# Performance work log

Hardware: AMD Instinct MI355X
Metric: run time of the kernel (lower is better)

The kernel has to match this reference:

```python
import jax, jax.numpy as jnp
import numpy as np


def setup_inputs() -> dict:
    key = jax.random.key(0)
    k1, k2, k3 = jax.random.split(key, 3)
    N = 100000
    E = 1600000
    d = 128
    indices = jax.random.randint(k1, (2, E), 0, N, dtype=jnp.int64)
    values = jax.random.uniform(k2, (E,), dtype=jnp.float32)
    b = jax.random.normal(k3, (N, d), dtype=jnp.float32)
    return {"indices": indices, "values": values, "b": b, "N": N, "layer_id": 0}


def reference(indices, values, b, N, layer_id):
    # Sparse COO matmul: out[r] = sum_{e: row[e]==r} values[e] * b[col[e]]
    row = indices[0]  # [E]
    col = indices[1]  # [E]
    contrib = values[:, None] * b[col]  # [E, d] gathered + scaled edge messages
    out = jax.ops.segment_sum(contrib, row, num_segments=N)  # [N, d]
    return out
```

## Files before the change

kernel.cpp:

```cpp
#include <hip/hip_runtime.h>


#define DIM 128
#define RPB 32
#define BLK 128
#define STAGE 768
#define CAP (STAGE + 7 * RPB)
#define NCH 256
#define MAXNB 4096

__device__ __forceinline__ unsigned short f2bf(float f) {
    unsigned u = __float_as_uint(f);
    return (unsigned short)((u + 0x7FFFu + ((u >> 16) & 1u)) >> 16);
}
__device__ __forceinline__ float4 ldbf4(const char* p) {
    ushort4 h = *reinterpret_cast<const ushort4*>(p);
    float4 r;
    r.x = __uint_as_float((unsigned)h.x << 16);
    r.y = __uint_as_float((unsigned)h.y << 16);
    r.z = __uint_as_float((unsigned)h.z << 16);
    r.w = __uint_as_float((unsigned)h.w << 16);
    return r;
}

__global__ __launch_bounds__(256) void spmm_atomic_kernel(
    const int* __restrict__ rows, const int* __restrict__ cols,
    const float* __restrict__ vals, const float* __restrict__ b,
    float* __restrict__ out, int E)
{
    long long t = (long long)blockIdx.x * blockDim.x + threadIdx.x;
    int e = (int)(t >> 5);
    if (e >= E) return;
    int j = ((int)t & 31) * 4;
    int r = rows[e]; int c = cols[e]; float v = vals[e];
    const float4 bv = *reinterpret_cast<const float4*>(b + (size_t)c * DIM + j);
    float* o = out + (size_t)r * DIM + j;
    atomicAdd(o + 0, v * bv.x);
    atomicAdd(o + 1, v * bv.y);
    atomicAdd(o + 2, v * bv.z);
    atomicAdd(o + 3, v * bv.w);
}

__global__ __launch_bounds__(256) void conv_count_kernel(
    const float* __restrict__ b, unsigned short* __restrict__ bh, int n4,
    const int* __restrict__ rows, int* __restrict__ ccount, int E)
{
    for (int i = blockIdx.x * blockDim.x + threadIdx.x; i < n4;
         i += gridDim.x * blockDim.x) {
        float4 v = reinterpret_cast<const float4*>(b)[i];
        ushort4 h;
        h.x = f2bf(v.x); h.y = f2bf(v.y); h.z = f2bf(v.z); h.w = f2bf(v.w);
        reinterpret_cast<ushort4*>(bh)[i] = h;
    }
    __shared__ int hist[MAXNB];
    for (int i = threadIdx.x; i < MAXNB; i += 256) hist[i] = 0;
    __syncthreads();
    int chunk = (E + NCH - 1) / NCH;
    int s = blockIdx.x * chunk;
    int e = min(s + chunk, E);
    for (int i = s + threadIdx.x; i < e; i += 256)
        atomicAdd(&hist[rows[i] >> 5], 1);
    __syncthreads();
    for (int i = threadIdx.x; i < MAXNB; i += 256)
        if (hist[i]) atomicAdd(&ccount[i], hist[i]);
}

__global__ __launch_bounds__(1024) void coarse_scan_kernel(
    const int* __restrict__ ccount, int* __restrict__ coffsets,
    int* __restrict__ ccursor, int NB, int E)
{
    __shared__ int s[1024];
    int t = threadIdx.x;
    int i0 = 4 * t;
    int a0 = (i0     < NB) ? ccount[i0]     : 0;
    int a1 = (i0 + 1 < NB) ? ccount[i0 + 1] : 0;
    int a2 = (i0 + 2 < NB) ? ccount[i0 + 2] : 0;
    int a3 = (i0 + 3 < NB) ? ccount[i0 + 3] : 0;
    int sum4 = a0 + a1 + a2 + a3;
    s[t] = sum4;
    __syncthreads();
    for (int off = 1; off < 1024; off <<= 1) {
        int x = (t >= off) ? s[t - off] : 0;
        __syncthreads();
        s[t] += x;
        __syncthreads();
    }
    int excl = s[t] - sum4;
    if (i0     < NB) { coffsets[i0]     = excl;                ccursor[i0]     = excl; }
    if (i0 + 1 < NB) { coffsets[i0 + 1] = excl + a0;           ccursor[i0 + 1] = excl + a0; }
    if (i0 + 2 < NB) { coffsets[i0 + 2] = excl + a0 + a1;      ccursor[i0 + 2] = excl + a0 + a1; }
    if (i0 + 3 < NB) { coffsets[i0 + 3] = excl + a0 + a1 + a2; ccursor[i0 + 3] = excl + a0 + a1 + a2; }
    if (t == 0) coffsets[NB] = E;
}

__global__ __launch_bounds__(256) void partition_kernel(
    const int* __restrict__ rows, const int* __restrict__ cols,
    const float* __restrict__ vals, int* __restrict__ ccursor,
    unsigned long long* __restrict__ pairs, int E)
{
    __shared__ int hist[MAXNB];
    __shared__ int base[MAXNB];
    for (int i = threadIdx.x; i < MAXNB; i += 256) hist[i] = 0;
    __syncthreads();
    int chunk = (E + NCH - 1) / NCH;
    int s = blockIdx.x * chunk;
    int e = min(s + chunk, E);
    for (int i = s + threadIdx.x; i < e; i += 256)
        atomicAdd(&hist[rows[i] >> 5], 1);
    __syncthreads();
    for (int i = threadIdx.x; i < MAXNB; i += 256) {
        int c = hist[i];
        base[i] = c ? atomicAdd(&ccursor[i], c) : 0;
        hist[i] = 0;
    }
    __syncthreads();
    for (int i = s + threadIdx.x; i < e; i += 256) {
        int r = rows[i];
        int cb = r >> 5;
        int pos = base[cb] + atomicAdd(&hist[cb], 1);
        unsigned long long p =
            ((unsigned long long)(unsigned)__float_as_int(vals[i]) << 32) |
            (unsigned)((cols[i] << 5) | (r & (RPB - 1)));
        pairs[pos] = p;
    }
}

template<bool BF16>
__global__ __launch_bounds__(BLK) void bucket_accum_kernel(
    const int* __restrict__ coffsets,
    const unsigned long long* __restrict__ pairs,
    const void* __restrict__ bmat, float* __restrict__ out, int N)
{
    __shared__ int2 svec[CAP];
    __shared__ int fcnt[RPB];
    __shared__ int foff[RPB + 1];
    __shared__ int stmp[RPB];

    int cb = blockIdx.x;
    int cstart = coffsets[cb];
    int Mtot = coffsets[cb + 1] - cstart;
    int M = min(Mtot, STAGE);
    int t = threadIdx.x;

    unsigned long long ep0 = 0, ep1 = 0, ep2 = 0, ep3 = 0, ep4 = 0, ep5 = 0;
    {
        const unsigned long long* p = pairs + cstart;
        if (t         < M) ep0 = p[t];
        if (t + 128   < M) ep1 = p[t + 128];
        if (t + 256   < M) ep2 = p[t + 256];
        if (t + 384   < M) ep3 = p[t + 384];
        if (t + 512   < M) ep4 = p[t + 512];
        if (t + 640   < M) ep5 = p[t + 640];
    }
    for (int i = t; i < CAP; i += BLK) svec[i] = make_int2(0, 0);
    if (t < RPB) fcnt[t] = 0;
    __syncthreads();

    if (t         < M) atomicAdd(&fcnt[(int)(ep0 & (RPB - 1))], 1);
    if (t + 128   < M) atomicAdd(&fcnt[(int)(ep1 & (RPB - 1))], 1);
    if (t + 256   < M) atomicAdd(&fcnt[(int)(ep2 & (RPB - 1))], 1);
    if (t + 384   < M) atomicAdd(&fcnt[(int)(ep3 & (RPB - 1))], 1);
    if (t + 512   < M) atomicAdd(&fcnt[(int)(ep4 & (RPB - 1))], 1);
    if (t + 640   < M) atomicAdd(&fcnt[(int)(ep5 & (RPB - 1))], 1);
    __syncthreads();

    int pc = 0;
    if (t < RPB) { pc = (fcnt[t] + 7) & ~7; stmp[t] = pc; }
    __syncthreads();
    for (int off = 1; off < RPB; off <<= 1) {
        int x = 0;
        if (t < RPB && t >= off) x = stmp[t - off];
        __syncthreads();
        if (t < RPB) stmp[t] += x;
        __syncthreads();
    }
    if (t < RPB) {
        int excl = stmp[t] - pc;
        foff[t] = excl;
        fcnt[t] = excl;
    }
    if (t == RPB - 1) foff[RPB] = stmp[t];
    __syncthreads();

#define RANK_WRITE(EP, OFS)                                                  \
    if (t + (OFS) < M) {                                                     \
        unsigned lo = (unsigned)(EP & 0xffffffffu);                          \
        int pos = atomicAdd(&fcnt[(int)(lo & (RPB - 1))], 1);                \
        svec[pos] = make_int2((int)((lo & 0xffffffe0u) << (BF16 ? 3 : 4)),   \
                              (int)(EP >> 32));                              \
    }
    RANK_WRITE(ep0, 0)   RANK_WRITE(ep1, 128) RANK_WRITE(ep2, 256)
    RANK_WRITE(ep3, 384) RANK_WRITE(ep4, 512) RANK_WRITE(ep5, 640)
#undef RANK_WRITE
    __syncthreads();

    int wid  = t >> 6;
    int lane = t & 63;
    int h    = lane >> 5;
    int sub  = lane & 31;
    const char* blh = (const char*)bmat + sub * (BF16 ? 8 : 16);

#define GATHER(DST, OFS)                                                     \
    if constexpr (BF16) DST = ldbf4(blh + (OFS));                            \
    else DST = *reinterpret_cast<const float4*>(blh + (OFS));

#define FMA4(EV, CV)                                                         \
    { float v = __int_as_float(EV.y);                                        \
      acc.x = fmaf(v, CV.x, acc.x); acc.y = fmaf(v, CV.y, acc.y);            \
      acc.z = fmaf(v, CV.z, acc.z); acc.w = fmaf(v, CV.w, acc.w); }

    for (int j = 0; j < 16; ++j) {
        int rl = wid * 16 + j;
        int rg = cb * RPB + rl;
        if (rg >= N) break;
        float4 acc = make_float4(0.f, 0.f, 0.f, 0.f);
        int ks = foff[rl], ke = foff[rl + 1];
        if (ks < ke) {
            int2 e0 = svec[ks + h],     e1 = svec[ks + 2 + h];
            int2 e2 = svec[ks + 4 + h], e3 = svec[ks + 6 + h];
            float4 c0, c1, c2, c3;
            GATHER(c0, e0.x) GATHER(c1, e1.x) GATHER(c2, e2.x) GATHER(c3, e3.x)
            for (int k = ks + 8; k < ke; k += 8) {
                int2 f0 = svec[k + h],     f1 = svec[k + 2 + h];
                int2 f2 = svec[k + 4 + h], f3 = svec[k + 6 + h];
                float4 d0, d1, d2, d3;
                GATHER(d0, f0.x) GATHER(d1, f1.x) GATHER(d2, f2.x) GATHER(d3, f3.x)
                __builtin_amdgcn_sched_barrier(0);
                FMA4(e0, c0) FMA4(e1, c1) FMA4(e2, c2) FMA4(e3, c3)
                e0 = f0; e1 = f1; e2 = f2; e3 = f3;
                c0 = d0; c1 = d1; c2 = d2; c3 = d3;
            }
            FMA4(e0, c0) FMA4(e1, c1) FMA4(e2, c2) FMA4(e3, c3)
        }
        if (h == 0) {
            for (int q = STAGE; q < Mtot; ++q) {
                unsigned long long p = pairs[cstart + q];
                if ((int)(p & (RPB - 1)) == rl) {
                    unsigned lo = (unsigned)(p & 0xffffffffu);
                    float v = __int_as_float((int)(p >> 32));
                    float4 bv;
                    GATHER(bv, (int)((lo & 0xffffffe0u) << (BF16 ? 3 : 4)))
                    acc.x = fmaf(v, bv.x, acc.x); acc.y = fmaf(v, bv.y, acc.y);
                    acc.z = fmaf(v, bv.z, acc.z); acc.w = fmaf(v, bv.w, acc.w);
                }
            }
        }
        acc.x += __shfl_xor(acc.x, 32);
        acc.y += __shfl_xor(acc.y, 32);
        acc.z += __shfl_xor(acc.z, 32);
        acc.w += __shfl_xor(acc.w, 32);
        if (h == 0)
            *reinterpret_cast<float4*>(out + (size_t)rg * DIM + sub * 4) = acc;
    }
#undef FMA4
#undef GATHER
}

extern "C" void kernel_launch(void* const* d_in, const int* in_sizes, int n_in,
                              void* d_out, int out_size, void* d_ws, size_t ws_size,
                              hipStream_t stream)
{
    const int*   indices = (const int*)d_in[0];
    const float* vals    = (const float*)d_in[1];
    const float* b       = (const float*)d_in[2];
    float*       out     = (float*)d_out;

    const int E = in_sizes[1];
    const int N = in_sizes[2] / DIM;
    const int* rows = indices;
    const int* cols = indices + E;

    const int NB = (N + RPB - 1) / RPB;

    size_t pairs_bytes = (size_t)E * 8;
    size_t bh_bytes    = (size_t)N * DIM * 2;
    size_t cnt_bytes   = ((size_t)NB * 3 + 1) * 4;
    size_t needed_f32  = pairs_bytes + cnt_bytes;
    size_t needed_bf16 = pairs_bytes + bh_bytes + cnt_bytes;

    if (ws_size < needed_f32 || NB > MAXNB || NB < 1 || E < 1) {
        hipMemsetAsync(d_out, 0, (size_t)out_size * sizeof(float), stream);
        if (E >= 1) {
            const long long total = (long long)E * 32;
            const int grid = (int)((total + 255) / 256);
            spmm_atomic_kernel<<<grid, 256, 0, stream>>>(rows, cols, vals, b, out, E);
        }
        return;
    }

    const bool use_bf16 = (ws_size >= needed_bf16);

    char* base = (char*)d_ws;
    unsigned long long* pairs = (unsigned long long*)base;
    size_t off = pairs_bytes;
    unsigned short* bh = nullptr;
    if (use_bf16) { bh = (unsigned short*)(base + off); off += bh_bytes; }
    int* ccount   = (int*)(base + off);
    int* coffsets = ccount + NB;
    int* ccursor  = coffsets + (NB + 1);

    hipMemsetAsync(ccount, 0, (size_t)NB * sizeof(int), stream);
    conv_count_kernel<<<NCH, 256, 0, stream>>>(
        b, bh, use_bf16 ? N * DIM / 4 : 0, rows, ccount, E);
    coarse_scan_kernel<<<1, 1024, 0, stream>>>(ccount, coffsets, ccursor, NB, E);
    partition_kernel<<<NCH, 256, 0, stream>>>(rows, cols, vals, ccursor, pairs, E);
    if (use_bf16)
        bucket_accum_kernel<true><<<NB, BLK, 0, stream>>>(coffsets, pairs, bh, out, N);
    else
        bucket_accum_kernel<false><<<NB, BLK, 0, stream>>>(coffsets, pairs, b, out, N);
}
```

Before: 152.3 us.

## Split edge partitioning into two-level radix scatter via superbuckets

Partitioning now runs in two passes: edges are first scattered into superbuckets of 1024 rows, then each superbucket is redistributed into 32-row buckets. The pair encoding widens the row field to 10 bits so the second pass can read the sub-bucket index. The aim is more local, better-coalesced scatter writes than a single scatter into thousands of buckets. The cost is an extra pass over the pair array, additional workspace, and an extra kernel launch.

```diff
diff --git a/kernel.cpp b/kernel.cpp
--- a/kernel.cpp
+++ b/kernel.cpp
@@ -7,7 +7,10 @@
 #define STAGE 768
 #define CAP (STAGE + 7 * RPB)
 #define NCH 256
+#define NCH1 1024
+#define PB2 8
 #define MAXNB 4096
+#define MAXNSB 128
 
 __device__ __forceinline__ unsigned short f2bf(float f) {
     unsigned u = __float_as_uint(f);
@@ -67,7 +70,7 @@
 
 __global__ __launch_bounds__(1024) void coarse_scan_kernel(
     const int* __restrict__ ccount, int* __restrict__ coffsets,
-    int* __restrict__ ccursor, int NB, int E)
+    int* __restrict__ ccursor, int* __restrict__ scursor, int NB, int E)
 {
     __shared__ int s[1024];
     int t = threadIdx.x;
@@ -90,10 +93,79 @@
     if (i0 + 1 < NB) { coffsets[i0 + 1] = excl + a0;           ccursor[i0 + 1] = excl + a0; }
     if (i0 + 2 < NB) { coffsets[i0 + 2] = excl + a0 + a1;      ccursor[i0 + 2] = excl + a0 + a1; }
     if (i0 + 3 < NB) { coffsets[i0 + 3] = excl + a0 + a1 + a2; ccursor[i0 + 3] = excl + a0 + a1 + a2; }
+    if ((i0 & 31) == 0 && i0 < NB) scursor[i0 >> 5] = excl;
     if (t == 0) coffsets[NB] = E;
 }
 
-__global__ __launch_bounds__(256) void partition_kernel(
+#define PACK(VAL, COL, ROW)                                                  \
+    (((unsigned long long)(unsigned)__float_as_int(VAL) << 32) |             \
+     (unsigned)(((COL) << 10) | ((ROW) & 1023)))
+
+__global__ __launch_bounds__(256) void partition1_kernel(
+    const int* __restrict__ rows, const int* __restrict__ cols,
+    const float* __restrict__ vals, int* __restrict__ scursor,
+    unsigned long long* __restrict__ pairs1, int E)
+{
+    __shared__ int hist[MAXNSB];
+    __shared__ int base[MAXNSB];
+    if (threadIdx.x < MAXNSB) hist[threadIdx.x] = 0;
+    __syncthreads();
+    int chunk = (E + NCH1 - 1) / NCH1;
+    int s = blockIdx.x * chunk;
+    int e = min(s + chunk, E);
+    for (int i = s + threadIdx.x; i < e; i += 256)
+        atomicAdd(&hist[rows[i] >> 10], 1);
+    __syncthreads();
+    if (threadIdx.x < MAXNSB) {
+        int c = hist[threadIdx.x];
+        base[threadIdx.x] = c ? atomicAdd(&scursor[threadIdx.x], c) : 0;
+        hist[threadIdx.x] = 0;
+    }
+    __syncthreads();
+    for (int i = s + threadIdx.x; i < e; i += 256) {
+        int r = rows[i];
+        int sb = r >> 10;
+        int pos = base[sb] + atomicAdd(&hist[sb], 1);
+        pairs1[pos] = PACK(vals[i], cols[i], r);
+    }
+}
+
+__global__ __launch_bounds__(256) void partition2_kernel(
+    const int* __restrict__ coffsets, int* __restrict__ ccursor,
+    const unsigned long long* __restrict__ pairs1,
+    unsigned long long* __restrict__ pairs2, int NB)
+{
+    int sb = blockIdx.x >> 3;
+    int q  = blockIdx.x & (PB2 - 1);
+    int b0 = sb * 32;
+    int b1 = min(b0 + 32, NB);
+    int sstart = coffsets[b0];
+    int len = coffsets[b1] - sstart;
+    int s = sstart + (int)((long long)len * q / PB2);
+    int e = sstart + (int)((long long)len * (q + 1) / PB2);
+
+    __shared__ int hist[32];
+    __shared__ int base[32];
+    if (threadIdx.x < 32) hist[threadIdx.x] = 0;
+    __syncthreads();
+    for (int i = s + threadIdx.x; i < e; i += 256)
+        atomicAdd(&hist[((unsigned)pairs1[i] >> 5) & 31], 1);
+    __syncthreads();
+    if (threadIdx.x < 32) {
+        int c = hist[threadIdx.x];
+        base[threadIdx.x] = c ? atomicAdd(&ccursor[b0 + threadIdx.x], c) : 0;
+        hist[threadIdx.x] = 0;
+    }
+    __syncthreads();
+    for (int i = s + threadIdx.x; i < e; i += 256) {
+        unsigned long long p = pairs1[i];
+        int sub = ((unsigned)p >> 5) & 31;
+        int pos = base[sub] + atomicAdd(&hist[sub], 1);
+        pairs2[pos] = p;
+    }
+}
+
+__global__ __launch_bounds__(256) void partition_single_kernel(
     const int* __restrict__ rows, const int* __restrict__ cols,
     const float* __restrict__ vals, int* __restrict__ ccursor,
     unsigned long long* __restrict__ pairs, int E)
@@ -118,10 +190,7 @@
         int r = rows[i];
         int cb = r >> 5;
         int pos = base[cb] + atomicAdd(&hist[cb], 1);
-        unsigned long long p =
-            ((unsigned long long)(unsigned)__float_as_int(vals[i]) << 32) |
-            (unsigned)((cols[i] << 5) | (r & (RPB - 1)));
-        pairs[pos] = p;
+        pairs[pos] = PACK(vals[i], cols[i], r);
     }
 }
 
@@ -156,12 +225,12 @@
     if (t < RPB) fcnt[t] = 0;
     __syncthreads();
 
-    if (t         < M) atomicAdd(&fcnt[(int)(ep0 & (RPB - 1))], 1);
-    if (t + 128   < M) atomicAdd(&fcnt[(int)(ep1 & (RPB - 1))], 1);
-    if (t + 256   < M) atomicAdd(&fcnt[(int)(ep2 & (RPB - 1))], 1);
-    if (t + 384   < M) atomicAdd(&fcnt[(int)(ep3 & (RPB - 1))], 1);
-    if (t + 512   < M) atomicAdd(&fcnt[(int)(ep4 & (RPB - 1))], 1);
-    if (t + 640   < M) atomicAdd(&fcnt[(int)(ep5 & (RPB - 1))], 1);
+    if (t         < M) atomicAdd(&fcnt[(int)(ep0 & 31u)], 1);
+    if (t + 128   < M) atomicAdd(&fcnt[(int)(ep1 & 31u)], 1);
+    if (t + 256   < M) atomicAdd(&fcnt[(int)(ep2 & 31u)], 1);
+    if (t + 384   < M) atomicAdd(&fcnt[(int)(ep3 & 31u)], 1);
+    if (t + 512   < M) atomicAdd(&fcnt[(int)(ep4 & 31u)], 1);
+    if (t + 640   < M) atomicAdd(&fcnt[(int)(ep5 & 31u)], 1);
     __syncthreads();
 
     int pc = 0;
@@ -185,8 +254,8 @@
 #define RANK_WRITE(EP, OFS)                                                  \
     if (t + (OFS) < M) {                                                     \
         unsigned lo = (unsigned)(EP & 0xffffffffu);                          \
-        int pos = atomicAdd(&fcnt[(int)(lo & (RPB - 1))], 1);                \
-        svec[pos] = make_int2((int)((lo & 0xffffffe0u) << (BF16 ? 3 : 4)),   \
+        int pos = atomicAdd(&fcnt[(int)(lo & 31u)], 1);                      \
+        svec[pos] = make_int2((int)((lo >> 10) << (BF16 ? 8 : 9)),           \
                               (int)(EP >> 32));                              \
     }
     RANK_WRITE(ep0, 0)   RANK_WRITE(ep1, 128) RANK_WRITE(ep2, 256)
@@ -235,11 +304,11 @@
         if (h == 0) {
             for (int q = STAGE; q < Mtot; ++q) {
                 unsigned long long p = pairs[cstart + q];
-                if ((int)(p & (RPB - 1)) == rl) {
+                if ((int)(p & 31u) == rl) {
                     unsigned lo = (unsigned)(p & 0xffffffffu);
                     float v = __int_as_float((int)(p >> 32));
                     float4 bv;
-                    GATHER(bv, (int)((lo & 0xffffffe0u) << (BF16 ? 3 : 4)))
+                    GATHER(bv, (int)((lo >> 10) << (BF16 ? 8 : 9)))
                     acc.x = fmaf(v, bv.x, acc.x); acc.y = fmaf(v, bv.y, acc.y);
                     acc.z = fmaf(v, bv.z, acc.z); acc.w = fmaf(v, bv.w, acc.w);
                 }
@@ -270,13 +339,15 @@
     const int* rows = indices;
     const int* cols = indices + E;
 
-    const int NB = (N + RPB - 1) / RPB;
+    const int NB  = (N + RPB - 1) / RPB;
+    const int NSB = (NB + 31) / 32;
 
     size_t pairs_bytes = (size_t)E * 8;
     size_t bh_bytes    = (size_t)N * DIM * 2;
-    size_t cnt_bytes   = ((size_t)NB * 3 + 1) * 4;
+    size_t cnt_bytes   = ((size_t)NB * 3 + 1 + NSB) * 4;
     size_t needed_f32  = pairs_bytes + cnt_bytes;
     size_t needed_bf16 = pairs_bytes + bh_bytes + cnt_bytes;
+    size_t needed_2lv  = needed_bf16 + pairs_bytes;
 
     if (ws_size < needed_f32 || NB > MAXNB || NB < 1 || E < 1) {
         hipMemsetAsync(d_out, 0, (size_t)out_size * sizeof(float), stream);
@@ -288,24 +359,37 @@
         return;
     }
 
-    const bool use_bf16 = (ws_size >= needed_bf16);
+    const bool use_bf16  = (ws_size >= needed_bf16);
+    const bool two_level = (ws_size >= needed_2lv);
 
     char* base = (char*)d_ws;
-    unsigned long long* pairs = (unsigned long long*)base;
+    unsigned long long* pairs2 = (unsigned long long*)base;
     size_t off = pairs_bytes;
     unsigned short* bh = nullptr;
     if (use_bf16) { bh = (unsigned short*)(base + off); off += bh_bytes; }
+    unsigned long long* pairs1 = nullptr;
+    if (two_level) { pairs1 = (unsigned long long*)(base + off); off += pairs_bytes; }
     int* ccount   = (int*)(base + off);
     int* coffsets = ccount + NB;
     int* ccursor  = coffsets + (NB + 1);
+    int* scursor  = ccursor + NB;
 
     hipMemsetAsync(ccount, 0, (size_t)NB * sizeof(int), stream);
     conv_count_kernel<<<NCH, 256, 0, stream>>>(
         b, bh, use_bf16 ? N * DIM / 4 : 0, rows, ccount, E);
-    coarse_scan_kernel<<<1, 1024, 0, stream>>>(ccount, coffsets, ccursor, NB, E);
-    partition_kernel<<<NCH, 256, 0, stream>>>(rows, cols, vals, ccursor, pairs, E);
+    coarse_scan_kernel<<<1, 1024, 0, stream>>>(
+        ccount, coffsets, ccursor, scursor, NB, E);
+    if (two_level) {
+        partition1_kernel<<<NCH1, 256, 0, stream>>>(
+            rows, cols, vals, scursor, pairs1, E);
+        partition2_kernel<<<NSB * PB2, 256, 0, stream>>>(
+            coffsets, ccursor, pairs1, pairs2, NB);
+    } else {
+        partition_single_kernel<<<NCH, 256, 0, stream>>>(
+            rows, cols, vals, ccursor, pairs2, E);
+    }
     if (use_bf16)
-        bucket_accum_kernel<true><<<NB, BLK, 0, stream>>>(coffsets, pairs, bh, out, N);
+        bucket_accum_kernel<true><<<NB, BLK, 0, stream>>>(coffsets, pairs2, bh, out, N);
     else
-        bucket_accum_kernel<false><<<NB, BLK, 0, stream>>>(coffsets, pairs, b, out, N);
-}
+        bucket_accum_kernel<false><<<NB, BLK, 0, stream>>>(coffsets, pairs2, b, out, N);
+}
```

Result: faster. 148.9 us (-2.2%).
